# Kernel tuning notes

Measured on AMD Instinct MI355X. Metric: run time of the kernel, lower is better.

The kernel has to match this reference:

```python
import jax, jax.numpy as jnp
import numpy as np

# Static configuration matching init_kwargs
LR_SHAPES = ((64, 64), (128, 128), (256, 256))
H0, W0 = LR_SHAPES[0]          # selected layer (layer_number = 0)
UP = (8, 8)                     # upscale factors -> output_dim = 64
OUT_DIM = UP[0] * UP[1]
KERNEL = (3, 3)
PAD = (1, 1)
BATCH = 64
WEIGHTS_IN = 189                # 9 + 36 + 144


def _unfold(x, kernel, stride, pad):
    """torch.F.unfold equivalent for NCHW input with C==1.
    x: (N, 1, H, W) -> (N, kh*kw, L) with row-major spatial positions."""
    patches = jax.lax.conv_general_dilated_patches(
        x,
        filter_shape=kernel,
        window_strides=stride,
        padding=((pad[0], pad[0]), (pad[1], pad[1])),
        dimension_numbers=('NCHW', 'OIHW', 'NCHW'),
    )  # (N, kh*kw, H_out, W_out)
    n, k, h, w = patches.shape
    return patches.reshape(n, k, h * w)


def setup_inputs() -> dict:
    key = jax.random.key(0)
    k0, k1, k2, kw = jax.random.split(key, 4)
    x0 = jax.random.normal(k0, (BATCH, 1, 64, 64), dtype=jnp.float32)
    x1 = jax.random.normal(k1, (BATCH, 1, 128, 128), dtype=jnp.float32)
    x2 = jax.random.normal(k2, (BATCH, 1, 256, 256), dtype=jnp.float32)
    # original uses uniform(-stdv, stdv) with tiny stdv; small-scale normal keeps
    # the softmax non-degenerate while matching the magnitude regime
    weight = jax.random.normal(kw, (WEIGHTS_IN, OUT_DIM), dtype=jnp.float32) * 0.01
    return {"x0": x0, "x1": x1, "x2": x2, "weight": weight}


def reference(x0, x1, x2, weight):
    xs = (x0, x1, x2)
    cols = []
    for j, (hj, wj) in enumerate(LR_SHAPES):
        s = (hj // H0, wj // W0)                       # scale vs selected layer
        f = (KERNEL[0] * s[0], KERNEL[1] * s[1])       # scaled kernel
        p = (PAD[0] * s[0], PAD[1] * s[1])             # scaled padding
        cols.append(_unfold(xs[j], f, s, p))           # (N, 9*s0*s1, L)
    X = jnp.concatenate(cols, axis=1)                  # (N, 189, L), L = H0*W0

    # per-pixel attention weights: matmul + ReLU + softmax
    logits = jax.nn.relu(jnp.einsum('nkl,ko->nlo', X, weight))  # (N, L, 64)
    soft = jax.nn.softmax(logits, axis=-1)                       # (N, L, 64)

    # reassemble: each LR pixel value scaled by its 64 attention weights (C==1)
    xsel = x0.reshape(x0.shape[0], H0 * W0)            # (N, L)
    out = xsel[:, :, None] * soft                      # (N, L, 64)

    # fold(kernel=1) == reshape to (N, 64, H0, W0)
    n = out.shape[0]
    out = out.transpose(0, 2, 1).reshape(n, OUT_DIM, H0, W0)

    # pixel shuffle -> (N, 1, H0*up0, W0*up1)
    out = out.reshape(n, 1, UP[0], UP[1], H0, W0)
    out = out.transpose(0, 1, 4, 2, 5, 3)
    return out.reshape(n, 1, H0 * UP[0], W0 * UP[1])
```

## Files before the change

### kernel.cpp

```cpp
#include <hip/hip_runtime.h>

typedef _Float16 f16;
typedef f16 f16x8 __attribute__((ext_vector_type(8)));
typedef f16 f16x4 __attribute__((ext_vector_type(4)));
typedef float f32x4 __attribute__((ext_vector_type(4)));

#define S0 28
#define S1 48
#define S2 92
#define T0OFF 0
#define T1OFF (19 * S0)
#define T2OFF (T1OFF + 36 * S1)
#define TILEH (T2OFF + 76 * S2)
#define SCRSTR 68
#define SMEM_BYTES 34816
#define LOG2E 1.4426950408889634f

__global__ void prep_wt(const float* __restrict__ W, f16* __restrict__ Wt) {
  const int f = blockIdx.x * 256 + threadIdx.x;
  const int s = f >> 8;
  const int t = (f >> 6) & 3;
  const int lane = f & 63;
  const int quad = lane >> 4, ln = lane & 15;
  const int n = t * 16 + ln;
  f16 vals[8];
  #pragma unroll
  for (int j = 0; j < 8; ++j) {
    int kp = s * 32 + quad * 8 + j;
    int orig = -1;
    if (kp < 16)      { int ki = kp >> 2, kj = kp & 3;                   if (ki < 3 && kj < 3) orig = 3*ki + kj; }
    else if (kp < 64) { int kk = kp - 16; int ki = kk >> 3, kj = kk & 7;  if (kj < 6)          orig = 9 + 6*ki + kj; }
    else              { int kk = kp - 64; int ki = kk >> 4, kj = kk & 15; if (kj < 12)         orig = 45 + 12*ki + kj; }
    vals[j] = (f16)((orig >= 0) ? W[orig * 64 + n] : 0.f);
  }
  *(f16x8*)(Wt + (size_t)f * 8) = *(const f16x8*)vals;
}

__global__ __launch_bounds__(256, 3) void fuse_kernel(
    const float* __restrict__ x0, const float* __restrict__ x1,
    const float* __restrict__ x2, const f16* __restrict__ Wt,
    float* __restrict__ out)
{
  __shared__ __align__(16) char smem_raw[SMEM_BYTES];
  f16*   tiles   = (f16*)smem_raw;
  float* scratch = (float*)smem_raw;

  const int tid  = threadIdx.x;
  const int bid  = blockIdx.x;
  const int nb   = bid >> 4;
  const int ty   = (bid >> 2) & 3;
  const int tx   = bid & 3;
  const int lane = tid & 63;
  const int wid  = tid >> 6;
  const int ln   = lane & 15;
  const int quad = lane >> 4;

  const f16* __restrict__ wfrag = Wt + (size_t)lane * 8;

  f32x4 v2[7];
  int   off2[7];
  bool  ok2[7];
  {
    const float* img = x2 + nb * 65536;
    #pragma unroll
    for (int i = 0; i < 7; ++i) {
      int idx = tid + 256 * i;
      int r  = idx / 22, c4 = idx - r * 22;
      int gy = ty * 64 - 4 + r;
      int gx = tx * 64 - 8 + 4 * c4;
      bool inb = (idx < 1672) && ((unsigned)gy < 256u) && ((unsigned)gx < 256u);
      v2[i]  = inb ? *(const f32x4*)(img + gy * 256 + gx) : (f32x4){0.f, 0.f, 0.f, 0.f};
      off2[i] = T2OFF + r * S2 + 4 * c4;
      ok2[i]  = (idx < 1672);
    }
  }

  {
    const float* img = x1 + nb * 16384;
    #pragma unroll
    for (int i = 0; i < 2; ++i) {
      int idx = tid + 256 * i;
      int r  = idx / 11, c4 = idx - r * 11;
      int gy = ty * 32 - 2 + r;
      int gx = tx * 32 - 4 + 4 * c4;
      bool inb = (idx < 396) && ((unsigned)gy < 128u) && ((unsigned)gx < 128u);
      f32x4 t = inb ? *(const f32x4*)(img + gy * 128 + gx) : (f32x4){0.f, 0.f, 0.f, 0.f};
      if (idx < 396) {
        f16x4 h; h[0] = (f16)t[0]; h[1] = (f16)t[1]; h[2] = (f16)t[2]; h[3] = (f16)t[3];
        *(f16x4*)&tiles[T1OFF + r * S1 + 4 * c4] = h;
      }
    }
  }
  {
    const float* img = x0 + nb * 4096;
    int idx = tid;
    int r  = idx / 6, c4 = idx - r * 6;
    int gy = ty * 16 - 1 + r;
    int gx = tx * 16 - 4 + 4 * c4;
    bool inb = (idx < 114) && ((unsigned)gy < 64u) && ((unsigned)gx < 64u);
    f32x4 t = inb ? *(const f32x4*)(img + gy * 64 + gx) : (f32x4){0.f, 0.f, 0.f, 0.f};
    if (idx < 114) {
      f16x4 h; h[0] = (f16)t[0]; h[1] = (f16)t[1]; h[2] = (f16)t[2]; h[3] = (f16)t[3];
      *(f16x4*)&tiles[T0OFF + r * S0 + 4 * c4] = h;
    }
  }

  float xs[4];
  #pragma unroll
  for (int cc = 0; cc < 4; ++cc)
    xs[cc] = x0[nb * 4096 + (ty * 16 + wid * 4 + cc) * 64 + tx * 16 + ln];

  __syncthreads();

  f32x4 acc[4][4];
  #pragma unroll
  for (int c = 0; c < 4; ++c)
    #pragma unroll
    for (int t = 0; t < 4; ++t)
      acc[c][t] = (f32x4){0.f, 0.f, 0.f, 0.f};

  {
    f16x8 bf[4];
    #pragma unroll
    for (int t = 0; t < 4; ++t)
      bf[t] = *(const f16x8*)(wfrag + t * 512);
    #pragma unroll
    for (int cc = 0; cc < 4; ++cc) {
      const int py = wid * 4 + cc;
      f16x8 a;
      if (quad < 2) {
        const int a0 = T0OFF + (py + 2 * quad) * S0 + ln + 3;
        #pragma unroll
        for (int j = 0; j < 4; ++j) a[j]     = tiles[a0 + j];
        #pragma unroll
        for (int j = 0; j < 4; ++j) a[4 + j] = tiles[a0 + S0 + j];
      } else {
        const int a1 = T1OFF + (2 * py + quad - 2) * S1 + 2 * ln + 2;
        #pragma unroll
        for (int j = 0; j < 8; ++j) a[j] = tiles[a1 + j];
      }
      #pragma unroll
      for (int t = 0; t < 4; ++t)
        acc[cc][t] = __builtin_amdgcn_mfma_f32_16x16x32_f16(a, bf[t], acc[cc][t], 0, 0, 0);
    }
  }
  {
    f16x8 bf[4];
    #pragma unroll
    for (int t = 0; t < 4; ++t)
      bf[t] = *(const f16x8*)(wfrag + (4 + t) * 512);
    #pragma unroll
    for (int cc = 0; cc < 4; ++cc) {
      const int py = wid * 4 + cc;
      const int a1 = T1OFF + (2 * py + 2 + quad) * S1 + 2 * ln + 2;
      f16x8 a;
      #pragma unroll
      for (int j = 0; j < 8; ++j) a[j] = tiles[a1 + j];
      #pragma unroll
      for (int t = 0; t < 4; ++t)
        acc[cc][t] = __builtin_amdgcn_mfma_f32_16x16x32_f16(a, bf[t], acc[cc][t], 0, 0, 0);
    }
  }

  #pragma unroll
  for (int i = 0; i < 7; ++i) {
    if (ok2[i]) {
      f16x4 h0; h0[0] = (f16)v2[i][0]; h0[1] = (f16)v2[i][1];
      h0[2] = (f16)v2[i][2]; h0[3] = (f16)v2[i][3];
      *(f16x4*)&tiles[off2[i]] = h0;
    }
  }
  __syncthreads();

  #pragma unroll 3
  for (int s = 2; s < 8; ++s) {
    f16x8 bf[4];
    #pragma unroll
    for (int t = 0; t < 4; ++t)
      bf[t] = *(const f16x8*)(wfrag + (s * 4 + t) * 512);
    #pragma unroll
    for (int cc = 0; cc < 4; ++cc) {
      const int py = wid * 4 + cc;
      const int b2 = T2OFF + (4 * py + 2 * (s - 2) + (quad >> 1)) * S2 + 4 * ln + 4 + 8 * (quad & 1);
      f16x4 lo = *(const f16x4*)&tiles[b2];
      f16x4 hi = *(const f16x4*)&tiles[b2 + 4];
      f16x8 a;
      a[0] = lo[0]; a[1] = lo[1]; a[2] = lo[2]; a[3] = lo[3];
      a[4] = hi[0]; a[5] = hi[1]; a[6] = hi[2]; a[7] = hi[3];
      #pragma unroll
      for (int t = 0; t < 4; ++t)
        acc[cc][t] = __builtin_amdgcn_mfma_f32_16x16x32_f16(a, bf[t], acc[cc][t], 0, 0, 0);
    }
  }

  __syncthreads();

  float* swp0 = scratch + wid * 16 * SCRSTR;
  float* swp1 = scratch + (4 + wid) * 16 * SCRSTR;
  #pragma unroll
  for (int cp = 0; cp < 2; ++cp) {
    const int c0 = 2 * cp, c1 = 2 * cp + 1;
    #pragma unroll
    for (int t = 0; t < 4; ++t)
      #pragma unroll
      for (int r = 0; r < 4; ++r) {
        swp0[(quad * 4 + r) * SCRSTR + t * 16 + ln] = fmaxf(acc[c0][t][r], 0.f);
        swp1[(quad * 4 + r) * SCRSTR + t * 16 + ln] = fmaxf(acc[c1][t][r], 0.f);
      }
    asm volatile("s_waitcnt lgkmcnt(0)" ::: "memory");

    f32x4 v0[4], v1[4];
    #pragma unroll
    for (int u = 0; u < 4; ++u) {
      v0[u] = *(const f32x4*)&swp0[ln * SCRSTR + quad * 16 + 4 * u];
      v1[u] = *(const f32x4*)&swp1[ln * SCRSTR + quad * 16 + 4 * u];
    }

    float m0 = 0.f, m1 = 0.f;
    #pragma unroll
    for (int u = 0; u < 4; ++u)
      #pragma unroll
      for (int e = 0; e < 4; ++e) {
        m0 = fmaxf(m0, v0[u][e]);
        m1 = fmaxf(m1, v1[u][e]);
      }
    m0 = fmaxf(m0, __shfl_xor(m0, 16));
    m1 = fmaxf(m1, __shfl_xor(m1, 16));
    m0 = fmaxf(m0, __shfl_xor(m0, 32));
    m1 = fmaxf(m1, __shfl_xor(m1, 32));

    float s0 = 0.f, s1 = 0.f;
    #pragma unroll
    for (int u = 0; u < 4; ++u)
      #pragma unroll
      for (int e = 0; e < 4; ++e) {
        float e0 = exp2f((v0[u][e] - m0) * LOG2E);
        float e1 = exp2f((v1[u][e] - m1) * LOG2E);
        v0[u][e] = e0; v1[u][e] = e1;
        s0 += e0; s1 += e1;
      }
    s0 += __shfl_xor(s0, 16);
    s1 += __shfl_xor(s1, 16);
    s0 += __shfl_xor(s0, 32);
    s1 += __shfl_xor(s1, 32);

    const float sc0 = xs[c0] / s0;
    const float sc1 = xs[c1] / s1;

    const int gx = tx * 16 + ln;
    {
      const int gy = ty * 16 + wid * 4 + c0;
      float* op = out + nb * 262144 + (gy * 8 + 2 * quad) * 512 + gx * 8;
      *(f32x4*)(op)           = v0[0] * sc0;
      *(f32x4*)(op + 4)       = v0[1] * sc0;
      *(f32x4*)(op + 512)     = v0[2] * sc0;
      *(f32x4*)(op + 512 + 4) = v0[3] * sc0;
    }
    {
      const int gy = ty * 16 + wid * 4 + c1;
      float* op = out + nb * 262144 + (gy * 8 + 2 * quad) * 512 + gx * 8;
      *(f32x4*)(op)           = v1[0] * sc1;
      *(f32x4*)(op + 4)       = v1[1] * sc1;
      *(f32x4*)(op + 512)     = v1[2] * sc1;
      *(f32x4*)(op + 512 + 4) = v1[3] * sc1;
    }
  }
}

extern "C" void kernel_launch(void* const* d_in, const int* in_sizes, int n_in,
                              void* d_out, int out_size, void* d_ws, size_t ws_size,
                              hipStream_t stream) {
  const float* x0 = (const float*)d_in[0];
  const float* x1 = (const float*)d_in[1];
  const float* x2 = (const float*)d_in[2];
  const float* W  = (const float*)d_in[3];
  float* outp     = (float*)d_out;
  f16* Wt         = (f16*)d_ws;

  prep_wt<<<dim3(8), dim3(256), 0, stream>>>(W, Wt);
  fuse_kernel<<<dim3(1024), dim3(256), 0, stream>>>(x0, x1, x2, Wt, outp);
}
```

Before: 117.7 us.

## Halve per-block tile, swap MFMA operands to drop LDS transpose, nontemporal stores

Each block now covers 8 LR rows instead of 16, so the grid doubles to 2048 blocks and occupancy rises to 6 blocks per CU through smaller LDS and accumulator footprints. The MFMA operands are swapped so accumulators come out transposed, which lets the softmax run directly in registers and removes the LDS scratch round-trip and its barrier. All tiles are loaded before a single barrier, and output writes use nontemporal stores. A block-index swizzle reorders the schedule, and the smaller tiles add halo reloading overhead.

```diff
diff --git a/kernel.cpp b/kernel.cpp
--- a/kernel.cpp
+++ b/kernel.cpp
@@ -9,11 +9,9 @@
 #define S1 48
 #define S2 92
 #define T0OFF 0
-#define T1OFF (19 * S0)
-#define T2OFF (T1OFF + 36 * S1)
-#define TILEH (T2OFF + 76 * S2)
-#define SCRSTR 68
-#define SMEM_BYTES 34816
+#define T1OFF (11 * S0)
+#define T2OFF (T1OFF + 20 * S1)
+#define TILEH (T2OFF + 40 * S2)
 #define LOG2E 1.4426950408889634f
 
 __global__ void prep_wt(const float* __restrict__ W, f16* __restrict__ Wt) {
@@ -36,19 +34,17 @@
   *(f16x8*)(Wt + (size_t)f * 8) = *(const f16x8*)vals;
 }
 
-__global__ __launch_bounds__(256, 3) void fuse_kernel(
+__global__ __launch_bounds__(256, 6) void fuse_kernel(
     const float* __restrict__ x0, const float* __restrict__ x1,
     const float* __restrict__ x2, const f16* __restrict__ Wt,
     float* __restrict__ out)
 {
-  __shared__ __align__(16) char smem_raw[SMEM_BYTES];
-  f16*   tiles   = (f16*)smem_raw;
-  float* scratch = (float*)smem_raw;
+  __shared__ __align__(16) f16 tiles[TILEH];
 
   const int tid  = threadIdx.x;
-  const int bid  = blockIdx.x;
-  const int nb   = bid >> 4;
-  const int ty   = (bid >> 2) & 3;
+  const int bid  = ((blockIdx.x & 7) << 8) | (blockIdx.x >> 3);
+  const int nb   = bid >> 5;
+  const int ty   = (bid >> 2) & 7;
   const int tx   = bid & 3;
   const int lane = tid & 63;
   const int wid  = tid >> 6;
@@ -57,64 +53,69 @@
 
   const f16* __restrict__ wfrag = Wt + (size_t)lane * 8;
 
-  f32x4 v2[7];
-  int   off2[7];
-  bool  ok2[7];
+  f32x4 v2[4];
+  int   off2[4];
+  bool  ok2[4];
   {
     const float* img = x2 + nb * 65536;
     #pragma unroll
-    for (int i = 0; i < 7; ++i) {
+    for (int i = 0; i < 4; ++i) {
       int idx = tid + 256 * i;
       int r  = idx / 22, c4 = idx - r * 22;
-      int gy = ty * 64 - 4 + r;
+      int gy = ty * 32 - 4 + r;
       int gx = tx * 64 - 8 + 4 * c4;
-      bool inb = (idx < 1672) && ((unsigned)gy < 256u) && ((unsigned)gx < 256u);
+      bool inb = (idx < 880) && ((unsigned)gy < 256u) && ((unsigned)gx < 256u);
       v2[i]  = inb ? *(const f32x4*)(img + gy * 256 + gx) : (f32x4){0.f, 0.f, 0.f, 0.f};
       off2[i] = T2OFF + r * S2 + 4 * c4;
-      ok2[i]  = (idx < 1672);
+      ok2[i]  = (idx < 880);
     }
   }
 
   {
     const float* img = x1 + nb * 16384;
-    #pragma unroll
-    for (int i = 0; i < 2; ++i) {
-      int idx = tid + 256 * i;
-      int r  = idx / 11, c4 = idx - r * 11;
-      int gy = ty * 32 - 2 + r;
-      int gx = tx * 32 - 4 + 4 * c4;
-      bool inb = (idx < 396) && ((unsigned)gy < 128u) && ((unsigned)gx < 128u);
-      f32x4 t = inb ? *(const f32x4*)(img + gy * 128 + gx) : (f32x4){0.f, 0.f, 0.f, 0.f};
-      if (idx < 396) {
-        f16x4 h; h[0] = (f16)t[0]; h[1] = (f16)t[1]; h[2] = (f16)t[2]; h[3] = (f16)t[3];
-        *(f16x4*)&tiles[T1OFF + r * S1 + 4 * c4] = h;
-      }
+    int idx = tid;
+    int r  = idx / 11, c4 = idx - r * 11;
+    int gy = ty * 16 - 2 + r;
+    int gx = tx * 32 - 4 + 4 * c4;
+    bool inb = (idx < 220) && ((unsigned)gy < 128u) && ((unsigned)gx < 128u);
+    f32x4 t = inb ? *(const f32x4*)(img + gy * 128 + gx) : (f32x4){0.f, 0.f, 0.f, 0.f};
+    if (idx < 220) {
+      f16x4 h; h[0] = (f16)t[0]; h[1] = (f16)t[1]; h[2] = (f16)t[2]; h[3] = (f16)t[3];
+      *(f16x4*)&tiles[T1OFF + r * S1 + 4 * c4] = h;
     }
   }
   {
     const float* img = x0 + nb * 4096;
     int idx = tid;
     int r  = idx / 6, c4 = idx - r * 6;
-    int gy = ty * 16 - 1 + r;
+    int gy = ty * 8 - 1 + r;
     int gx = tx * 16 - 4 + 4 * c4;
-    bool inb = (idx < 114) && ((unsigned)gy < 64u) && ((unsigned)gx < 64u);
+    bool inb = (idx < 66) && ((unsigned)gy < 64u) && ((unsigned)gx < 64u);
     f32x4 t = inb ? *(const f32x4*)(img + gy * 64 + gx) : (f32x4){0.f, 0.f, 0.f, 0.f};
-    if (idx < 114) {
+    if (idx < 66) {
       f16x4 h; h[0] = (f16)t[0]; h[1] = (f16)t[1]; h[2] = (f16)t[2]; h[3] = (f16)t[3];
       *(f16x4*)&tiles[T0OFF + r * S0 + 4 * c4] = h;
     }
   }
 
-  float xs[4];
-  #pragma unroll
-  for (int cc = 0; cc < 4; ++cc)
-    xs[cc] = x0[nb * 4096 + (ty * 16 + wid * 4 + cc) * 64 + tx * 16 + ln];
-
+  float xs[2];
+  #pragma unroll
+  for (int cc = 0; cc < 2; ++cc)
+    xs[cc] = x0[nb * 4096 + (ty * 8 + wid * 2 + cc) * 64 + tx * 16 + ln];
+
+  #pragma unroll
+  for (int i = 0; i < 4; ++i) {
+    if (ok2[i]) {
+      f16x4 h; h[0] = (f16)v2[i][0]; h[1] = (f16)v2[i][1];
+      h[2] = (f16)v2[i][2]; h[3] = (f16)v2[i][3];
+      *(f16x4*)&tiles[off2[i]] = h;
+    }
+  }
   __syncthreads();
 
-  f32x4 acc[4][4];
-  #pragma unroll
-  for (int c = 0; c < 4; ++c)
+  f32x4 acc[2][4];
+  #pragma unroll
+  for (int c = 0; c < 2; ++c)
     #pragma unroll
     for (int t = 0; t < 4; ++t)
       acc[c][t] = (f32x4){0.f, 0.f, 0.f, 0.f};
@@ -125,8 +126,8 @@
     for (int t = 0; t < 4; ++t)
       bf[t] = *(const f16x8*)(wfrag + t * 512);
     #pragma unroll
-    for (int cc = 0; cc < 4; ++cc) {
-      const int py = wid * 4 + cc;
+    for (int cc = 0; cc < 2; ++cc) {
+      const int py = wid * 2 + cc;
       f16x8 a;
       if (quad < 2) {
         const int a0 = T0OFF + (py + 2 * quad) * S0 + ln + 3;
@@ -141,7 +142,7 @@
       }
       #pragma unroll
       for (int t = 0; t < 4; ++t)
-        acc[cc][t] = __builtin_amdgcn_mfma_f32_16x16x32_f16(a, bf[t], acc[cc][t], 0, 0, 0);
+        acc[cc][t] = __builtin_amdgcn_mfma_f32_16x16x32_f16(bf[t], a, acc[cc][t], 0, 0, 0);
     }
   }
   {
@@ -150,28 +151,17 @@
     for (int t = 0; t < 4; ++t)
       bf[t] = *(const f16x8*)(wfrag + (4 + t) * 512);
     #pragma unroll
-    for (int cc = 0; cc < 4; ++cc) {
-      const int py = wid * 4 + cc;
+    for (int cc = 0; cc < 2; ++cc) {
+      const int py = wid * 2 + cc;
       const int a1 = T1OFF + (2 * py + 2 + quad) * S1 + 2 * ln + 2;
       f16x8 a;
       #pragma unroll
       for (int j = 0; j < 8; ++j) a[j] = tiles[a1 + j];
       #pragma unroll
       for (int t = 0; t < 4; ++t)
-        acc[cc][t] = __builtin_amdgcn_mfma_f32_16x16x32_f16(a, bf[t], acc[cc][t], 0, 0, 0);
-    }
-  }
-
-  #pragma unroll
-  for (int i = 0; i < 7; ++i) {
-    if (ok2[i]) {
-      f16x4 h0; h0[0] = (f16)v2[i][0]; h0[1] = (f16)v2[i][1];
-      h0[2] = (f16)v2[i][2]; h0[3] = (f16)v2[i][3];
-      *(f16x4*)&tiles[off2[i]] = h0;
-    }
-  }
-  __syncthreads();
-
+        acc[cc][t] = __builtin_amdgcn_mfma_f32_16x16x32_f16(bf[t], a, acc[cc][t], 0, 0, 0);
+    }
+  }
   #pragma unroll 3
   for (int s = 2; s < 8; ++s) {
     f16x8 bf[4];
@@ -179,8 +169,8 @@
     for (int t = 0; t < 4; ++t)
       bf[t] = *(const f16x8*)(wfrag + (s * 4 + t) * 512);
     #pragma unroll
-    for (int cc = 0; cc < 4; ++cc) {
-      const int py = wid * 4 + cc;
+    for (int cc = 0; cc < 2; ++cc) {
+      const int py = wid * 2 + cc;
       const int b2 = T2OFF + (4 * py + 2 * (s - 2) + (quad >> 1)) * S2 + 4 * ln + 4 + 8 * (quad & 1);
       f16x4 lo = *(const f16x4*)&tiles[b2];
       f16x4 hi = *(const f16x4*)&tiles[b2 + 4];
@@ -189,80 +179,47 @@
       a[4] = hi[0]; a[5] = hi[1]; a[6] = hi[2]; a[7] = hi[3];
       #pragma unroll
       for (int t = 0; t < 4; ++t)
-        acc[cc][t] = __builtin_amdgcn_mfma_f32_16x16x32_f16(a, bf[t], acc[cc][t], 0, 0, 0);
-    }
-  }
-
-  __syncthreads();
-
-  float* swp0 = scratch + wid * 16 * SCRSTR;
-  float* swp1 = scratch + (4 + wid) * 16 * SCRSTR;
-  #pragma unroll
-  for (int cp = 0; cp < 2; ++cp) {
-    const int c0 = 2 * cp, c1 = 2 * cp + 1;
+        acc[cc][t] = __builtin_amdgcn_mfma_f32_16x16x32_f16(bf[t], a, acc[cc][t], 0, 0, 0);
+    }
+  }
+
+  const int gx8 = (tx * 16 + ln) * 8;
+  #pragma unroll
+  for (int cc = 0; cc < 2; ++cc) {
+    float v[4][4];
+    float m = 0.f;
     #pragma unroll
     for (int t = 0; t < 4; ++t)
       #pragma unroll
       for (int r = 0; r < 4; ++r) {
-        swp0[(quad * 4 + r) * SCRSTR + t * 16 + ln] = fmaxf(acc[c0][t][r], 0.f);
-        swp1[(quad * 4 + r) * SCRSTR + t * 16 + ln] = fmaxf(acc[c1][t][r], 0.f);
+        float x = fmaxf(acc[cc][t][r], 0.f);
+        v[t][r] = x;
+        m = fmaxf(m, x);
       }
-    asm volatile("s_waitcnt lgkmcnt(0)" ::: "memory");
-
-    f32x4 v0[4], v1[4];
-    #pragma unroll
-    for (int u = 0; u < 4; ++u) {
-      v0[u] = *(const f32x4*)&swp0[ln * SCRSTR + quad * 16 + 4 * u];
-      v1[u] = *(const f32x4*)&swp1[ln * SCRSTR + quad * 16 + 4 * u];
-    }
-
-    float m0 = 0.f, m1 = 0.f;
-    #pragma unroll
-    for (int u = 0; u < 4; ++u)
-      #pragma unroll
-      for (int e = 0; e < 4; ++e) {
-        m0 = fmaxf(m0, v0[u][e]);
-        m1 = fmaxf(m1, v1[u][e]);
+    m = fmaxf(m, __shfl_xor(m, 16));
+    m = fmaxf(m, __shfl_xor(m, 32));
+
+    float sden = 0.f;
+    #pragma unroll
+    for (int t = 0; t < 4; ++t)
+      #pragma unroll
+      for (int r = 0; r < 4; ++r) {
+        float e = exp2f((v[t][r] - m) * LOG2E);
+        v[t][r] = e;
+        sden += e;
       }
-    m0 = fmaxf(m0, __shfl_xor(m0, 16));
-    m1 = fmaxf(m1, __shfl_xor(m1, 16));
-    m0 = fmaxf(m0, __shfl_xor(m0, 32));
-    m1 = fmaxf(m1, __shfl_xor(m1, 32));
-
-    float s0 = 0.f, s1 = 0.f;
-    #pragma unroll
-    for (int u = 0; u < 4; ++u)
-      #pragma unroll
-      for (int e = 0; e < 4; ++e) {
-        float e0 = exp2f((v0[u][e] - m0) * LOG2E);
-        float e1 = exp2f((v1[u][e] - m1) * LOG2E);
-        v0[u][e] = e0; v1[u][e] = e1;
-        s0 += e0; s1 += e1;
-      }
-    s0 += __shfl_xor(s0, 16);
-    s1 += __shfl_xor(s1, 16);
-    s0 += __shfl_xor(s0, 32);
-    s1 += __shfl_xor(s1, 32);
-
-    const float sc0 = xs[c0] / s0;
-    const float sc1 = xs[c1] / s1;
-
-    const int gx = tx * 16 + ln;
-    {
-      const int gy = ty * 16 + wid * 4 + c0;
-      float* op = out + nb * 262144 + (gy * 8 + 2 * quad) * 512 + gx * 8;
-      *(f32x4*)(op)           = v0[0] * sc0;
-      *(f32x4*)(op + 4)       = v0[1] * sc0;
-      *(f32x4*)(op + 512)     = v0[2] * sc0;
-      *(f32x4*)(op + 512 + 4) = v0[3] * sc0;
-    }
-    {
-      const int gy = ty * 16 + wid * 4 + c1;
-      float* op = out + nb * 262144 + (gy * 8 + 2 * quad) * 512 + gx * 8;
-      *(f32x4*)(op)           = v1[0] * sc1;
-      *(f32x4*)(op + 4)       = v1[1] * sc1;
-      *(f32x4*)(op + 512)     = v1[2] * sc1;
-      *(f32x4*)(op + 512 + 4) = v1[3] * sc1;
+    sden += __shfl_xor(sden, 16);
+    sden += __shfl_xor(sden, 32);
+
+    const float sc = xs[cc] / sden;
+    const int gy = ty * 8 + wid * 2 + cc;
+    float* op = out + nb * 262144 + (gy * 8 + (quad >> 1)) * 512 + gx8 + 4 * (quad & 1);
+    #pragma unroll
+    for (int t = 0; t < 4; ++t) {
+      f32x4 w;
+      w[0] = v[t][0] * sc; w[1] = v[t][1] * sc;
+      w[2] = v[t][2] * sc; w[3] = v[t][3] * sc;
+      __builtin_nontemporal_store(w, (f32x4*)(op + t * 1024));
     }
   }
 }
@@ -278,5 +235,5 @@
   f16* Wt         = (f16*)d_ws;
 
   prep_wt<<<dim3(8), dim3(256), 0, stream>>>(W, Wt);
-  fuse_kernel<<<dim3(1024), dim3(256), 0, stream>>>(x0, x1, x2, Wt, outp);
+  fuse_kernel<<<dim3(2048), dim3(256), 0, stream>>>(x0, x1, x2, Wt, outp);
 }
```

Result: faster. 108.5 us (-7.8%).
